# Optimization experiments

Measured on AMD Instinct MI355X. Metric: run time of the kernel, lower is better.

## Reference

```python
import jax, jax.numpy as jnp
import numpy as np

E = 1024
H = 16
HD = E // H


def setup_inputs() -> dict:
    key = jax.random.key(0)
    k1, k2, k3, k4, k5 = jax.random.split(key, 5)
    x = jax.random.normal(k1, (2, 2048, E), dtype=jnp.float32)
    s = 1.0 / np.sqrt(E)
    qkv_w = jax.random.uniform(k2, (3 * E, E), jnp.float32, -s, s)
    qkv_b = jax.random.uniform(k3, (3 * E,), jnp.float32, -s, s)
    o_w = jax.random.uniform(k4, (E, E), jnp.float32, -s, s)
    o_b = jax.random.uniform(k5, (E,), jnp.float32, -s, s)
    return {"x": x, "qkv_w": qkv_w, "qkv_b": qkv_b, "o_w": o_w, "o_b": o_b}


def reference(x, qkv_w, qkv_b, o_w, o_b):
    B, T, _ = x.shape
    # qkv projection (torch Linear: x @ W.T + b)
    qkv = x @ qkv_w.T + qkv_b  # [B,T,3E]
    q, k, v = jnp.split(qkv, 3, axis=-1)
    # [B,H,T,HD]
    q = q.reshape(B, T, H, HD).transpose(0, 2, 1, 3)
    k = k.reshape(B, T, H, HD).transpose(0, 2, 1, 3)
    v = v.reshape(B, T, H, HD).transpose(0, 2, 1, 3)
    scores = jnp.einsum('bhqd,bhkd->bhqk', q, k) / np.sqrt(HD)
    causal = jnp.tril(jnp.ones((T, T), dtype=bool))
    scores = jnp.where(causal, scores, -jnp.inf)
    attn = jax.nn.softmax(scores, axis=-1)  # dropout disabled (eval mode)
    y = jnp.einsum('bhqk,bhkd->bhqd', attn, v)
    y = y.transpose(0, 2, 1, 3).reshape(B, T, E)
    return y @ o_w.T + o_b
```

## Files before the change

kernel.cpp:

```cpp
#include <hip/hip_runtime.h>
#include <hip/hip_bf16.h>
#include <math.h>

#define BATCH 2
#define SEQ   2048
#define EMB   1024
#define NH    16
#define HD    64
#define M_ROWS (BATCH * SEQ)

typedef __attribute__((ext_vector_type(8))) short bf16x8;
typedef __attribute__((ext_vector_type(4))) float f32x4;

__device__ __forceinline__ ushort f2bf(float f) {
    unsigned u = __float_as_uint(f);
    unsigned lsb = (u >> 16) & 1u;
    u += 0x7fffu + lsb;
    return (ushort)(u >> 16);
}

__device__ __forceinline__ unsigned cvt_pk_bf16(float lo, float hi) {
    unsigned r;
    asm("v_cvt_pk_bf16_f32 %0, %1, %2" : "=v"(r) : "v"(lo), "v"(hi));
    return r;
}

__device__ __forceinline__ void gload_lds16(const void* g, void* l) {
    __builtin_amdgcn_global_load_lds(
        (const __attribute__((address_space(1))) unsigned int*)g,
        (__attribute__((address_space(3))) unsigned int*)l, 16, 0, 0);
}

__global__ __launch_bounds__(256) void cvt3_f32_bf16(
    const float* __restrict__ s1, const float* __restrict__ s2,
    const float* __restrict__ s3, ushort* __restrict__ out,
    int n1, int n2)
{
    int i = (blockIdx.x * 256 + threadIdx.x) * 4;
    const float* src;
    int off;
    if (i < n1)            { src = s1; off = i; }
    else if (i < n1 + n2)  { src = s2; off = i - n1; }
    else                   { src = s3; off = i - n1 - n2; }
    float4 v = *reinterpret_cast<const float4*>(&src[off]);
    uint2 pk;
    pk.x = cvt_pk_bf16(v.x, v.y);
    pk.y = cvt_pk_bf16(v.z, v.w);
    *reinterpret_cast<uint2*>(&out[i]) = pk;
}

template <int MODE>
__global__ __launch_bounds__(256) void gemm_mfma_abt(
    const ushort* __restrict__ A, const ushort* __restrict__ B,
    const float* __restrict__ bias, float* __restrict__ Cout,
    ushort* __restrict__ qkb, ushort* __restrict__ vtb,
    int M, int N, int K)
{
    __shared__ ushort Al[128 * 64];
    __shared__ ushort Bl[128 * 64];

    const int tid  = threadIdx.x;
    const int lane = tid & 63;
    const int wave = tid >> 6;
    const int wr   = wave >> 1;
    const int wc   = wave & 1;
    const int l15  = lane & 15;
    const int l4   = lane >> 4;
    const int m0   = blockIdx.y * 128;
    const int n0   = blockIdx.x * 128;

    f32x4 acc[4][4];
#pragma unroll
    for (int m = 0; m < 4; ++m)
#pragma unroll
        for (int n = 0; n < 4; ++n)
#pragma unroll
            for (int r = 0; r < 4; ++r) acc[m][n][r] = 0.f;

    for (int k0 = 0; k0 < K; k0 += 64) {
#pragma unroll
        for (int it = 0; it < 4; ++it) {
            int chunk = tid + it * 256;
            int row = chunk >> 3;
            int kc  = (chunk & 7) * 8;
            gload_lds16(&A[(size_t)(m0 + row) * K + k0 + kc], &Al[chunk * 8]);
            gload_lds16(&B[(size_t)(n0 + row) * K + k0 + kc], &Bl[chunk * 8]);
        }
        __syncthreads();

#pragma unroll
        for (int kk = 0; kk < 2; ++kk) {
            const int ko = kk * 32 + l4 * 8;
            bf16x8 a[4], b[4];
#pragma unroll
            for (int m = 0; m < 4; ++m)
                a[m] = *reinterpret_cast<const bf16x8*>(
                    &Al[(wr * 64 + m * 16 + l15) * 64 + ko]);
#pragma unroll
            for (int n = 0; n < 4; ++n)
                b[n] = *reinterpret_cast<const bf16x8*>(
                    &Bl[(wc * 64 + n * 16 + l15) * 64 + ko]);
            __builtin_amdgcn_s_setprio(1);
#pragma unroll
            for (int m = 0; m < 4; ++m)
#pragma unroll
                for (int n = 0; n < 4; ++n)
                    acc[m][n] = __builtin_amdgcn_mfma_f32_16x16x32_bf16(
                        a[m], b[n], acc[m][n], 0, 0, 0);
            __builtin_amdgcn_s_setprio(0);
        }
        __syncthreads();
    }

#pragma unroll
    for (int n = 0; n < 4; ++n) {
        const int col = n0 + wc * 64 + n * 16 + l15;
        const float bv = bias[col];
        if (MODE == 0) {
#pragma unroll
            for (int m = 0; m < 4; ++m) {
                const int row0 = m0 + wr * 64 + m * 16 + l4 * 4;
#pragma unroll
                for (int r = 0; r < 4; ++r)
                    Cout[(size_t)(row0 + r) * N + col] = acc[m][n][r] + bv;
            }
        } else if (col < 2 * EMB) {
#pragma unroll
            for (int m = 0; m < 4; ++m) {
                const int row0 = m0 + wr * 64 + m * 16 + l4 * 4;
#pragma unroll
                for (int r = 0; r < 4; ++r)
                    qkb[(size_t)(row0 + r) * 2048 + col] = f2bf(acc[m][n][r] + bv);
            }
        } else {
            const int h = (col - 2 * EMB) >> 6;
            const int d = col & 63;
#pragma unroll
            for (int m = 0; m < 4; ++m) {
                const int row0 = m0 + wr * 64 + m * 16 + l4 * 4;
                const int bb = row0 >> 11;
                const int t  = row0 & 2047;
                uint2 pk;
                pk.x = cvt_pk_bf16(acc[m][n][0] + bv, acc[m][n][1] + bv);
                pk.y = cvt_pk_bf16(acc[m][n][2] + bv, acc[m][n][3] + bv);
                *reinterpret_cast<uint2*>(
                    &vtb[((size_t)(bb * 16 + h) * 64 + d) * 2048 + t]) = pk;
            }
        }
    }
}

__global__ __launch_bounds__(256) void attn_mfma(
    const ushort* __restrict__ qk, const ushort* __restrict__ vt,
    ushort* __restrict__ y)
{
    __shared__ alignas(16) ushort Kl[2][4096];
    __shared__ alignas(16) ushort Vl[2][4096];
    __shared__ alignas(16) ushort QP[8192];

    const int tid  = threadIdx.x;
    const int lane = tid & 63;
    const int w    = tid >> 6;
    const int l15  = lane & 15;
    const int l4   = lane >> 4;

    const int id  = blockIdx.x;
    const int xcd = id & 7;
    const int s   = (id >> 3) & 15;
    const int g   = id >> 7;
    const int bh  = xcd * 4 + g;
    const int qt  = (g < 2) ? (15 - s) : s;
    const int b   = bh >> 4;
    const int h   = bh & 15;

    const ushort* qbase = qk + (size_t)b * SEQ * 2048 + h * HD;
    const ushort* kbase = qbase + EMB;
    const ushort* vbase = vt + (size_t)bh * HD * SEQ;

    const int swz   = (l15 & 7) << 4;
    const int koff0 = ((l4 * 16) ^ swz) >> 1;
    const int koff1 = ((64 + l4 * 16) ^ swz) >> 1;

#pragma unroll
    for (int it = 0; it < 4; ++it) {
        int i = tid + it * 256;
        int r = i >> 3;
        int c = ((i & 7) ^ (r & 7)) << 3;
        gload_lds16(qbase + (size_t)(qt * 128 + r) * 2048 + c, &QP[i * 8]);
    }
#pragma unroll
    for (int it = 0; it < 2; ++it) {
        int i = tid + it * 256;
        int r = i >> 3;
        int c = ((i & 7) ^ (r & 7)) << 3;
        gload_lds16(kbase + (size_t)r * 2048 + c, &Kl[0][i * 8]);
    }
#pragma unroll
    for (int it = 0; it < 2; ++it) {
        int i = tid + it * 256;
        int d = i >> 3;
        int c = ((i & 7) ^ (d & 7)) << 3;
        gload_lds16(vbase + (size_t)d * 2048 + c, &Vl[0][i * 8]);
    }
    __syncthreads();

    const int qrow0 = (w * 32 + l15) * 64;
    const int qrow1 = (w * 32 + 16 + l15) * 64;
    const bf16x8 qf00 = *reinterpret_cast<const bf16x8*>(&QP[qrow0 + koff0]);
    const bf16x8 qf01 = *reinterpret_cast<const bf16x8*>(&QP[qrow0 + koff1]);
    const bf16x8 qf10 = *reinterpret_cast<const bf16x8*>(&QP[qrow1 + koff0]);
    const bf16x8 qf11 = *reinterpret_cast<const bf16x8*>(&QP[qrow1 + koff1]);

    const short OBF = (short)0x3F80;
    const bf16x8 ones = {OBF, OBF, OBF, OBF, OBF, OBF, OBF, OBF};

    f32x4 o0[4], o1[4];
#pragma unroll
    for (int n = 0; n < 4; ++n)
#pragma unroll
        for (int r = 0; r < 4; ++r) { o0[n][r] = 0.f; o1[n][r] = 0.f; }
    f32x4 lacc0 = {0.f, 0.f, 0.f, 0.f};
    f32x4 lacc1 = {0.f, 0.f, 0.f, 0.f};
    float m0 = -3.0e38f;
    float m1 = -3.0e38f;

    const float BETA = 0.18033688f;
    const int nkv = 2 * qt + 2;

    for (int kk = 0; kk < nkv; ++kk) {
        const int p = kk & 1;

        if (kk < nkv - 1) {
#pragma unroll
            for (int it = 0; it < 2; ++it) {
                int i = tid + it * 256;
                int r = i >> 3;
                int c = ((i & 7) ^ (r & 7)) << 3;
                gload_lds16(kbase + (size_t)((kk + 1) * 64 + r) * 2048 + c,
                            &Kl[p ^ 1][i * 8]);
            }
#pragma unroll
            for (int it = 0; it < 2; ++it) {
                int i = tid + it * 256;
                int d = i >> 3;
                int c = ((i & 7) ^ (d & 7)) << 3;
                gload_lds16(vbase + (size_t)d * 2048 + (kk + 1) * 64 + c,
                            &Vl[p ^ 1][i * 8]);
            }
        }

        bf16x8 kf[4][2];
#pragma unroll
        for (int n = 0; n < 4; ++n) {
            kf[n][0] = *reinterpret_cast<const bf16x8*>(
                &Kl[p][(n * 16 + l15) * 64 + koff0]);
            kf[n][1] = *reinterpret_cast<const bf16x8*>(
                &Kl[p][(n * 16 + l15) * 64 + koff1]);
        }

        f32x4 s0[4], s1[4];
        __builtin_amdgcn_s_setprio(1);
#pragma unroll
        for (int n = 0; n < 4; ++n) {
            f32x4 z0 = {0.f, 0.f, 0.f, 0.f};
            z0 = __builtin_amdgcn_mfma_f32_16x16x32_bf16(kf[n][0], qf00, z0, 0, 0, 0);
            s0[n] = __builtin_amdgcn_mfma_f32_16x16x32_bf16(kf[n][1], qf01, z0, 0, 0, 0);
            f32x4 z1 = {0.f, 0.f, 0.f, 0.f};
            z1 = __builtin_amdgcn_mfma_f32_16x16x32_bf16(kf[n][0], qf10, z1, 0, 0, 0);
            s1[n] = __builtin_amdgcn_mfma_f32_16x16x32_bf16(kf[n][1], qf11, z1, 0, 0, 0);
        }
        __builtin_amdgcn_s_setprio(0);

        bf16x8 vf[4][2];
#pragma unroll
        for (int n = 0; n < 4; ++n) {
            vf[n][0] = *reinterpret_cast<const bf16x8*>(
                &Vl[p][(n * 16 + l15) * 64 + koff0]);
            vf[n][1] = *reinterpret_cast<const bf16x8*>(
                &Vl[p][(n * 16 + l15) * 64 + koff1]);
        }

        if (kk >= nkv - 2) {
            const int q0 = qt * 128 + w * 32 + l15;
            const int q1 = q0 + 16;
#pragma unroll
            for (int n = 0; n < 4; ++n)
#pragma unroll
                for (int r = 0; r < 4; ++r) {
                    int kg = kk * 64 + n * 16 + l4 * 4 + r;
                    if (kg > q0) s0[n][r] = -3.0e38f;
                    if (kg > q1) s1[n][r] = -3.0e38f;
                }
        }

        float pm0, pm1;
        {
            float a0 = fmaxf(fmaxf(s0[0][0], s0[0][1]), fmaxf(s0[0][2], s0[0][3]));
            float a1 = fmaxf(fmaxf(s0[1][0], s0[1][1]), fmaxf(s0[1][2], s0[1][3]));
            float a2 = fmaxf(fmaxf(s0[2][0], s0[2][1]), fmaxf(s0[2][2], s0[2][3]));
            float a3 = fmaxf(fmaxf(s0[3][0], s0[3][1]), fmaxf(s0[3][2], s0[3][3]));
            pm0 = fmaxf(fmaxf(a0, a1), fmaxf(a2, a3)) * BETA;
            float b0 = fmaxf(fmaxf(s1[0][0], s1[0][1]), fmaxf(s1[0][2], s1[0][3]));
            float b1 = fmaxf(fmaxf(s1[1][0], s1[1][1]), fmaxf(s1[1][2], s1[1][3]));
            float b2 = fmaxf(fmaxf(s1[2][0], s1[2][1]), fmaxf(s1[2][2], s1[2][3]));
            float b3 = fmaxf(fmaxf(s1[3][0], s1[3][1]), fmaxf(s1[3][2], s1[3][3]));
            pm1 = fmaxf(fmaxf(b0, b1), fmaxf(b2, b3)) * BETA;
        }

        if (__any((pm0 > m0 + 8.0f) || (pm1 > m1 + 8.0f))) {
            float tm0 = fmaxf(pm0, __shfl_xor(pm0, 16));
            tm0 = fmaxf(tm0, __shfl_xor(tm0, 32));
            float tm1 = fmaxf(pm1, __shfl_xor(pm1, 16));
            tm1 = fmaxf(tm1, __shfl_xor(tm1, 32));
            float mn0 = fmaxf(m0, tm0);
            float al0 = exp2f(m0 - mn0);
            m0 = mn0;
            float mn1 = fmaxf(m1, tm1);
            float al1 = exp2f(m1 - mn1);
            m1 = mn1;
            float a00 = __shfl(al0, l4 * 4 + 0, 16);
            float a01 = __shfl(al0, l4 * 4 + 1, 16);
            float a02 = __shfl(al0, l4 * 4 + 2, 16);
            float a03 = __shfl(al0, l4 * 4 + 3, 16);
            float a10 = __shfl(al1, l4 * 4 + 0, 16);
            float a11 = __shfl(al1, l4 * 4 + 1, 16);
            float a12 = __shfl(al1, l4 * 4 + 2, 16);
            float a13 = __shfl(al1, l4 * 4 + 3, 16);
            lacc0[0] *= a00; lacc0[1] *= a01; lacc0[2] *= a02; lacc0[3] *= a03;
            lacc1[0] *= a10; lacc1[1] *= a11; lacc1[2] *= a12; lacc1[3] *= a13;
#pragma unroll
            for (int n = 0; n < 4; ++n) {
                o0[n][0] *= a00; o0[n][1] *= a01; o0[n][2] *= a02; o0[n][3] *= a03;
                o1[n][0] *= a10; o1[n][1] *= a11; o1[n][2] *= a12; o1[n][3] *= a13;
            }
        }

#pragma unroll
        for (int n = 0; n < 4; ++n) {
            float pa = exp2f(fmaf(s0[n][0], BETA, -m0));
            float pb = exp2f(fmaf(s0[n][1], BETA, -m0));
            float pc = exp2f(fmaf(s0[n][2], BETA, -m0));
            float pd = exp2f(fmaf(s0[n][3], BETA, -m0));
            uint2 pk;
            pk.x = cvt_pk_bf16(pa, pb);
            pk.y = cvt_pk_bf16(pc, pd);
            *reinterpret_cast<uint2*>(
                &QP[qrow0 + (((n * 32 + l4 * 8) ^ swz) >> 1)]) = pk;
            pa = exp2f(fmaf(s1[n][0], BETA, -m1));
            pb = exp2f(fmaf(s1[n][1], BETA, -m1));
            pc = exp2f(fmaf(s1[n][2], BETA, -m1));
            pd = exp2f(fmaf(s1[n][3], BETA, -m1));
            pk.x = cvt_pk_bf16(pa, pb);
            pk.y = cvt_pk_bf16(pc, pd);
            *reinterpret_cast<uint2*>(
                &QP[qrow1 + (((n * 32 + l4 * 8) ^ swz) >> 1)]) = pk;
        }

        bf16x8 pf00 = *reinterpret_cast<const bf16x8*>(&QP[qrow0 + koff0]);
        bf16x8 pf01 = *reinterpret_cast<const bf16x8*>(&QP[qrow0 + koff1]);
        bf16x8 pf10 = *reinterpret_cast<const bf16x8*>(&QP[qrow1 + koff0]);
        bf16x8 pf11 = *reinterpret_cast<const bf16x8*>(&QP[qrow1 + koff1]);
        __builtin_amdgcn_s_setprio(1);
        lacc0 = __builtin_amdgcn_mfma_f32_16x16x32_bf16(pf00, ones, lacc0, 0, 0, 0);
        lacc0 = __builtin_amdgcn_mfma_f32_16x16x32_bf16(pf01, ones, lacc0, 0, 0, 0);
        lacc1 = __builtin_amdgcn_mfma_f32_16x16x32_bf16(pf10, ones, lacc1, 0, 0, 0);
        lacc1 = __builtin_amdgcn_mfma_f32_16x16x32_bf16(pf11, ones, lacc1, 0, 0, 0);
#pragma unroll
        for (int n = 0; n < 4; ++n) {
            o0[n] = __builtin_amdgcn_mfma_f32_16x16x32_bf16(pf00, vf[n][0], o0[n], 0, 0, 0);
            o0[n] = __builtin_amdgcn_mfma_f32_16x16x32_bf16(pf01, vf[n][1], o0[n], 0, 0, 0);
            o1[n] = __builtin_amdgcn_mfma_f32_16x16x32_bf16(pf10, vf[n][0], o1[n], 0, 0, 0);
            o1[n] = __builtin_amdgcn_mfma_f32_16x16x32_bf16(pf11, vf[n][1], o1[n], 0, 0, 0);
        }
        __builtin_amdgcn_s_setprio(0);
        __syncthreads();
    }

#pragma unroll
    for (int r = 0; r < 4; ++r) {
        float inv0 = 1.f / lacc0[r];
        float inv1 = 1.f / lacc1[r];
        int row0 = qt * 128 + w * 32 + l4 * 4 + r;
        int row1 = row0 + 16;
#pragma unroll
        for (int n = 0; n < 4; ++n) {
            y[(size_t)(b * SEQ + row0) * EMB + h * HD + n * 16 + l15] =
                f2bf(o0[n][r] * inv0);
            y[(size_t)(b * SEQ + row1) * EMB + h * HD + n * 16 + l15] =
                f2bf(o1[n][r] * inv1);
        }
    }
}

extern "C" void kernel_launch(void* const* d_in, const int* in_sizes, int n_in,
                              void* d_out, int out_size, void* d_ws, size_t ws_size,
                              hipStream_t stream)
{
    const float* x     = (const float*)d_in[0];
    const float* qkv_w = (const float*)d_in[1];
    const float* qkv_b = (const float*)d_in[2];
    const float* o_w   = (const float*)d_in[3];
    const float* o_b   = (const float*)d_in[4];
    float* out = (float*)d_out;

    ushort* xb    = (ushort*)d_ws;
    ushort* wqkvb = xb    + (size_t)M_ROWS * EMB;
    ushort* owb   = wqkvb + (size_t)3 * EMB * EMB;
    ushort* qkb   = owb   + (size_t)EMB * EMB;
    ushort* vtb   = qkb   + (size_t)M_ROWS * 2 * EMB;
    ushort* ybb   = vtb   + (size_t)32 * HD * SEQ;

    {
        int n1 = M_ROWS * EMB;
        int n2 = 3 * EMB * EMB;
        int ntot = n1 + n2 + EMB * EMB;
        cvt3_f32_bf16<<<ntot / 1024, 256, 0, stream>>>(
            x, qkv_w, o_w, xb, n1, n2);
    }

    {
        dim3 grid(3 * EMB / 128, M_ROWS / 128);
        gemm_mfma_abt<1><<<grid, 256, 0, stream>>>(
            xb, wqkvb, qkv_b, nullptr, qkb, vtb, M_ROWS, 3 * EMB, EMB);
    }

    {
        attn_mfma<<<512, 256, 0, stream>>>(qkb, vtb, ybb);
    }

    {
        dim3 grid(EMB / 128, M_ROWS / 128);
        gemm_mfma_abt<0><<<grid, 256, 0, stream>>>(
            ybb, owb, o_b, out, nullptr, nullptr, M_ROWS, EMB, EMB);
    }
}
```

Baseline: 134.5 us.

## Process two KV tiles per barrier with four-slot LDS ring buffer

The attention loop now loads two 64-key K/V tiles per iteration into a four-slot LDS ring and processes both tiles before a single __syncthreads, halving barriers and doubling prefetch distance. Swizzled P-store offsets are precomputed into a small array. LDS use grows from about 48KB to about 80KB per block, which may reduce occupancy. The register footprint of the unrolled two-tile body also rises.

```diff
diff --git a/kernel.cpp b/kernel.cpp
--- a/kernel.cpp
+++ b/kernel.cpp
@@ -154,8 +154,8 @@
     const ushort* __restrict__ qk, const ushort* __restrict__ vt,
     ushort* __restrict__ y)
 {
-    __shared__ alignas(16) ushort Kl[2][4096];
-    __shared__ alignas(16) ushort Vl[2][4096];
+    __shared__ alignas(16) ushort Kl[4][4096];
+    __shared__ alignas(16) ushort Vl[4][4096];
     __shared__ alignas(16) ushort QP[8192];
 
     const int tid  = threadIdx.x;
@@ -194,6 +194,7 @@
         int r = i >> 3;
         int c = ((i & 7) ^ (r & 7)) << 3;
         gload_lds16(kbase + (size_t)r * 2048 + c, &Kl[0][i * 8]);
+        gload_lds16(kbase + (size_t)(64 + r) * 2048 + c, &Kl[1][i * 8]);
     }
 #pragma unroll
     for (int it = 0; it < 2; ++it) {
@@ -201,6 +202,7 @@
         int d = i >> 3;
         int c = ((i & 7) ^ (d & 7)) << 3;
         gload_lds16(vbase + (size_t)d * 2048 + c, &Vl[0][i * 8]);
+        gload_lds16(vbase + (size_t)d * 2048 + 64 + c, &Vl[1][i * 8]);
     }
     __syncthreads();
 
@@ -211,6 +213,10 @@
     const bf16x8 qf10 = *reinterpret_cast<const bf16x8*>(&QP[qrow1 + koff0]);
     const bf16x8 qf11 = *reinterpret_cast<const bf16x8*>(&QP[qrow1 + koff1]);
 
+    int pso[4];
+#pragma unroll
+    for (int n = 0; n < 4; ++n) pso[n] = ((n * 32 + l4 * 8) ^ swz) >> 1;
+
     const short OBF = (short)0x3F80;
     const bf16x8 ones = {OBF, OBF, OBF, OBF, OBF, OBF, OBF, OBF};
 
@@ -227,37 +233,15 @@
     const float BETA = 0.18033688f;
     const int nkv = 2 * qt + 2;
 
-    for (int kk = 0; kk < nkv; ++kk) {
-        const int p = kk & 1;
-
-        if (kk < nkv - 1) {
-#pragma unroll
-            for (int it = 0; it < 2; ++it) {
-                int i = tid + it * 256;
-                int r = i >> 3;
-                int c = ((i & 7) ^ (r & 7)) << 3;
-                gload_lds16(kbase + (size_t)((kk + 1) * 64 + r) * 2048 + c,
-                            &Kl[p ^ 1][i * 8]);
-            }
-#pragma unroll
-            for (int it = 0; it < 2; ++it) {
-                int i = tid + it * 256;
-                int d = i >> 3;
-                int c = ((i & 7) ^ (d & 7)) << 3;
-                gload_lds16(vbase + (size_t)d * 2048 + (kk + 1) * 64 + c,
-                            &Vl[p ^ 1][i * 8]);
-            }
-        }
-
+    auto computeTile = [&](const ushort* Kb, const ushort* Vb, int kkt) {
         bf16x8 kf[4][2];
 #pragma unroll
         for (int n = 0; n < 4; ++n) {
             kf[n][0] = *reinterpret_cast<const bf16x8*>(
-                &Kl[p][(n * 16 + l15) * 64 + koff0]);
+                &Kb[(n * 16 + l15) * 64 + koff0]);
             kf[n][1] = *reinterpret_cast<const bf16x8*>(
-                &Kl[p][(n * 16 + l15) * 64 + koff1]);
-        }
-
+                &Kb[(n * 16 + l15) * 64 + koff1]);
+        }
         f32x4 s0[4], s1[4];
         __builtin_amdgcn_s_setprio(1);
 #pragma unroll
@@ -275,19 +259,19 @@
 #pragma unroll
         for (int n = 0; n < 4; ++n) {
             vf[n][0] = *reinterpret_cast<const bf16x8*>(
-                &Vl[p][(n * 16 + l15) * 64 + koff0]);
+                &Vb[(n * 16 + l15) * 64 + koff0]);
             vf[n][1] = *reinterpret_cast<const bf16x8*>(
-                &Vl[p][(n * 16 + l15) * 64 + koff1]);
-        }
-
-        if (kk >= nkv - 2) {
+                &Vb[(n * 16 + l15) * 64 + koff1]);
+        }
+
+        if (kkt >= nkv - 2) {
             const int q0 = qt * 128 + w * 32 + l15;
             const int q1 = q0 + 16;
 #pragma unroll
             for (int n = 0; n < 4; ++n)
 #pragma unroll
                 for (int r = 0; r < 4; ++r) {
-                    int kg = kk * 64 + n * 16 + l4 * 4 + r;
+                    int kg = kkt * 64 + n * 16 + l4 * 4 + r;
                     if (kg > q0) s0[n][r] = -3.0e38f;
                     if (kg > q1) s1[n][r] = -3.0e38f;
                 }
@@ -344,16 +328,14 @@
             uint2 pk;
             pk.x = cvt_pk_bf16(pa, pb);
             pk.y = cvt_pk_bf16(pc, pd);
-            *reinterpret_cast<uint2*>(
-                &QP[qrow0 + (((n * 32 + l4 * 8) ^ swz) >> 1)]) = pk;
+            *reinterpret_cast<uint2*>(&QP[qrow0 + pso[n]]) = pk;
             pa = exp2f(fmaf(s1[n][0], BETA, -m1));
             pb = exp2f(fmaf(s1[n][1], BETA, -m1));
             pc = exp2f(fmaf(s1[n][2], BETA, -m1));
             pd = exp2f(fmaf(s1[n][3], BETA, -m1));
             pk.x = cvt_pk_bf16(pa, pb);
             pk.y = cvt_pk_bf16(pc, pd);
-            *reinterpret_cast<uint2*>(
-                &QP[qrow1 + (((n * 32 + l4 * 8) ^ swz) >> 1)]) = pk;
+            *reinterpret_cast<uint2*>(&QP[qrow1 + pso[n]]) = pk;
         }
 
         bf16x8 pf00 = *reinterpret_cast<const bf16x8*>(&QP[qrow0 + koff0]);
@@ -373,6 +355,36 @@
             o1[n] = __builtin_amdgcn_mfma_f32_16x16x32_bf16(pf11, vf[n][1], o1[n], 0, 0, 0);
         }
         __builtin_amdgcn_s_setprio(0);
+    };
+
+    for (int kk = 0; kk < nkv; kk += 2) {
+        if (kk + 2 < nkv) {
+            const int b2 = (kk + 2) & 3;
+            const int b3 = (kk + 3) & 3;
+#pragma unroll
+            for (int it = 0; it < 2; ++it) {
+                int i = tid + it * 256;
+                int r = i >> 3;
+                int c = ((i & 7) ^ (r & 7)) << 3;
+                gload_lds16(kbase + (size_t)((kk + 2) * 64 + r) * 2048 + c,
+                            &Kl[b2][i * 8]);
+                gload_lds16(kbase + (size_t)((kk + 3) * 64 + r) * 2048 + c,
+                            &Kl[b3][i * 8]);
+            }
+#pragma unroll
+            for (int it = 0; it < 2; ++it) {
+                int i = tid + it * 256;
+                int d = i >> 3;
+                int c = ((i & 7) ^ (d & 7)) << 3;
+                gload_lds16(vbase + (size_t)d * 2048 + (kk + 2) * 64 + c,
+                            &Vl[b2][i * 8]);
+                gload_lds16(vbase + (size_t)d * 2048 + (kk + 3) * 64 + c,
+                            &Vl[b3][i * 8]);
+            }
+        }
+
+        computeTile(Kl[kk & 3], Vl[kk & 3], kk);
+        computeTile(Kl[(kk + 1) & 3], Vl[(kk + 1) & 3], kk + 1);
         __syncthreads();
     }
 
```

After: 129.2 us. 1.04x faster.
